# Kernel optimization log

Measured on AMD Instinct MI355X. Metric: run time of the kernel, lower is better.

Reference implementation:

```python
import jax, jax.numpy as jnp
import numpy as np

N_NODES = 100000
N_EDGES = 1000000
IN_F, HID_F, OUT_F = 128, 128, 16


def setup_inputs() -> dict:
    key = jax.random.key(0)
    ks = jax.random.split(key, 8)
    x = jax.random.normal(ks[0], (N_NODES, IN_F), dtype=jnp.float32)
    src = jax.random.randint(ks[1], (N_EDGES,), 0, N_NODES, dtype=jnp.int64)
    dst = jax.random.randint(ks[2], (N_EDGES,), 0, N_NODES, dtype=jnp.int64)
    s = 1.0 / np.sqrt(HID_F)
    W1 = jax.random.normal(ks[3], (IN_F, HID_F), dtype=jnp.float32) * s
    W2 = jax.random.normal(ks[4], (HID_F, HID_F), dtype=jnp.float32) * s
    W3 = jax.random.normal(ks[5], (HID_F, HID_F), dtype=jnp.float32) * s
    W4 = jax.random.normal(ks[6], (HID_F, HID_F), dtype=jnp.float32) * s
    W5 = jax.random.normal(ks[7], (HID_F, OUT_F), dtype=jnp.float32) * s
    return {
        "x": x, "src": src, "dst": dst,
        "W1": W1, "b1": jnp.zeros((HID_F,), jnp.float32),
        "W2": W2, "b2": jnp.zeros((HID_F,), jnp.float32),
        "W3": W3, "b3": jnp.zeros((HID_F,), jnp.float32),
        "W4": W4, "b4": jnp.zeros((HID_F,), jnp.float32),
        "W5": W5, "b5": jnp.zeros((OUT_F,), jnp.float32),
    }


def reference(x, src, dst, W1, b1, W2, b2, W3, b3, W4, b4, W5, b5):
    N = x.shape[0]
    # in-degree per destination node (static graph, computed once)
    deg = jax.ops.segment_sum(jnp.ones_like(dst, dtype=x.dtype), dst, num_segments=N)
    inv = (1.0 / (deg + 1.0))[:, None]  # gcn aggregator normalizer: 1/(deg_in+1)

    def sage_gcn(h, W, b):
        # h_neigh[v] = (h[v] + sum_{u->v} h[u]) / (deg_in(v)+1); then linear
        agg = (h + jax.ops.segment_sum(h[src], dst, num_segments=N)) * inv
        return agg @ W + b

    h = jax.nn.relu(sage_gcn(x, W1, b1))
    h = jax.nn.relu(sage_gcn(h, W2, b2))
    h = jax.nn.relu(sage_gcn(h, W3, b3))
    h = jax.nn.relu(sage_gcn(h, W4, b4))
    h = sage_gcn(h, W5, b5)
    return jax.nn.log_softmax(h, axis=-1)
```

## Files before the change

### kernel.cpp

```cpp
#include <hip/hip_runtime.h>
#include <hip/hip_bf16.h>

#define NNODES 100000
#define NEDGES 1000000
#define HID 128
#define OUTF 16
#define NB 16
#define BCAP 81920
#define KB 64

typedef __attribute__((ext_vector_type(8))) short short8;
typedef __attribute__((ext_vector_type(4))) float floatx4;
typedef unsigned int uint32;
typedef unsigned short ushort16;

__device__ __forceinline__ float blo(uint32 u) { return __uint_as_float(u << 16); }
__device__ __forceinline__ float bhi(uint32 u) { return __uint_as_float(u & 0xffff0000u); }
__device__ __forceinline__ ushort16 f2b(float f) {
    __hip_bfloat16 h = __float2bfloat16(f);
    return *reinterpret_cast<ushort16*>(&h);
}


__global__ __launch_bounds__(256) void bucketize(const int* __restrict__ src,
                                                 const int* __restrict__ dst,
                                                 int* __restrict__ counts,
                                                 int* __restrict__ bcursor,
                                                 int2* __restrict__ stage, int E) {
    __shared__ int cnt[NB];
    __shared__ int base[NB];
    int t = threadIdx.x;
    int e = blockIdx.x * 256 + t;
    if (t < NB) cnt[t] = 0;
    __syncthreads();
    int s = 0, d = 0, b = 0, r = 0;
    bool valid = e < E;
    if (valid) {
        s = src[e];
        d = dst[e];
        atomicAdd(&counts[d], 1);
        b = (int)((unsigned)(d * NB) / (unsigned)NNODES);
        r = atomicAdd(&cnt[b], 1);
    }
    __syncthreads();
    if (t < NB) base[t] = atomicAdd(&bcursor[t], cnt[t]);
    __syncthreads();
    if (valid) {
        int pos = base[b] + r;
        if (pos < BCAP) stage[(size_t)b * BCAP + pos] = make_int2(s, d);
    }
}

__global__ __launch_bounds__(256) void fill2(const int2* __restrict__ stage,
                                             const int* __restrict__ bcursor,
                                             const int* __restrict__ offs,
                                             int* __restrict__ cursor,
                                             int* __restrict__ csr) {
    int blk = blockIdx.x;
    int b = (blk & 7) + 8 * ((blk >> 3) & 1);
    int slot = blk >> 4;
    int cntb = min(bcursor[b], BCAP);
    int per = (cntb + KB - 1) / KB;
    int s0 = slot * per;
    int s1 = min(s0 + per, cntb);
    const int2* st = stage + (size_t)b * BCAP;
    for (int i = s0 + threadIdx.x; i < s1; i += 256) {
        int2 sd = st[i];
        int p = atomicAdd(&cursor[sd.y], 1);
        csr[offs[sd.y] + p] = sd.x;
    }
}

__global__ void scan1(const int* __restrict__ counts, int* __restrict__ offs,
                      int* __restrict__ bsum, int N) {
    __shared__ int tmp[256];
    int t = threadIdx.x;
    int i = blockIdx.x * 256 + t;
    int v = (i < N) ? counts[i] : 0;
    tmp[t] = v;
    __syncthreads();
    for (int d = 1; d < 256; d <<= 1) {
        int add = (t >= d) ? tmp[t - d] : 0;
        __syncthreads();
        tmp[t] += add;
        __syncthreads();
    }
    if (i < N) offs[i] = tmp[t] - v;
    if (t == 255) bsum[blockIdx.x] = tmp[255];
}

__global__ void scan2(int* __restrict__ bsum, int nb) {
    __shared__ int tmp[512];
    int t = threadIdx.x;
    int v = (t < nb) ? bsum[t] : 0;
    tmp[t] = v;
    __syncthreads();
    for (int d = 1; d < 512; d <<= 1) {
        int add = (t >= d) ? tmp[t - d] : 0;
        __syncthreads();
        tmp[t] += add;
        __syncthreads();
    }
    if (t < nb) bsum[t] = tmp[t] - v;
}

__global__ void scan3(int* __restrict__ offs, const int* __restrict__ bsum,
                      const int* __restrict__ counts, float* __restrict__ inv,
                      int N, int E) {
    int i = blockIdx.x * 256 + threadIdx.x;
    if (i < N) {
        offs[i] += bsum[blockIdx.x];
        inv[i] = 1.0f / (float)(counts[i] + 1);
    }
    if (i == 0) offs[N] = E;
}


__global__ void pack_w(const float* __restrict__ W, ushort16* __restrict__ Wp) {
    int b = blockIdx.x;
    int lane = threadIdx.x;
    int nt = b >> 2, ks = b & 3;
    int n = nt * 16 + (lane & 15);
    int kbase = ks * 32 + ((lane >> 4) << 3);
    ushort16 tmp[8];
#pragma unroll
    for (int i = 0; i < 8; i++) tmp[i] = f2b(W[(size_t)(kbase + i) * HID + n]);
    *(uint4*)&Wp[((size_t)b * 64 + lane) * 8] = *(uint4*)tmp;
}


template <int AF32>
__global__ __launch_bounds__(256) void gemm_mfma(const void* __restrict__ Av,
                                                 const ushort16* __restrict__ Wp,
                                                 ushort16* __restrict__ Z, int M) {
    __shared__ __align__(16) ushort16 Wl[32 * 64 * 8];
    int t = threadIdx.x;
    const uint4* wp4 = (const uint4*)Wp;
    uint4* wl4 = (uint4*)Wl;
#pragma unroll
    for (int p = 0; p < 8; p++) wl4[t + p * 256] = wp4[t + p * 256];
    __syncthreads();

    int wv = t >> 6, lane = t & 63;
    int row = blockIdx.x * 64 + wv * 16 + (lane & 15);
    int rowc = min(row, M - 1);
    int kb = (lane >> 4) << 3;

    short8 a[4];
    if (AF32) {
        const float* A = (const float*)Av;
#pragma unroll
        for (int ks = 0; ks < 4; ks++) {
            const float* p = A + (size_t)rowc * HID + ks * 32 + kb;
            floatx4 lo = *(const floatx4*)p;
            floatx4 hi = *(const floatx4*)(p + 4);
            union { short8 s; ushort16 u[8]; } cv;
            cv.u[0] = f2b(lo.x); cv.u[1] = f2b(lo.y); cv.u[2] = f2b(lo.z); cv.u[3] = f2b(lo.w);
            cv.u[4] = f2b(hi.x); cv.u[5] = f2b(hi.y); cv.u[6] = f2b(hi.z); cv.u[7] = f2b(hi.w);
            a[ks] = cv.s;
        }
    } else {
        const ushort16* A = (const ushort16*)Av;
#pragma unroll
        for (int ks = 0; ks < 4; ks++)
            a[ks] = *(const short8*)(A + (size_t)rowc * HID + ks * 32 + kb);
    }

    floatx4 acc[8];
#pragma unroll
    for (int nt = 0; nt < 8; nt++) acc[nt] = (floatx4){0.f, 0.f, 0.f, 0.f};

#pragma unroll
    for (int nt = 0; nt < 8; nt++) {
#pragma unroll
        for (int ks = 0; ks < 4; ks++) {
            short8 b = *(const short8*)&Wl[(size_t)(((nt << 2) | ks) * 64 + lane) * 8];
            acc[nt] = __builtin_amdgcn_mfma_f32_16x16x32_bf16(a[ks], b, acc[nt], 0, 0, 0);
        }
    }

    int orow = blockIdx.x * 64 + wv * 16 + ((lane >> 4) << 2);
    int col = lane & 15;
#pragma unroll
    for (int i = 0; i < 4; i++) {
        int r = orow + i;
        if (r < M) {
#pragma unroll
            for (int nt = 0; nt < 8; nt++)
                Z[(size_t)r * HID + nt * 16 + col] = f2b(acc[nt][i]);
        }
    }
}


__global__ __launch_bounds__(256) void agg_bf16(const uint32* __restrict__ Z,
                                                const int* __restrict__ offs,
                                                const int* __restrict__ csr,
                                                const float* __restrict__ inv,
                                                const float* __restrict__ bias,
                                                uint32* __restrict__ H, int N) {
    int v = (blockIdx.x * blockDim.x + threadIdx.x) >> 6;
    int lane = threadIdx.x & 63;
    if (v >= N) return;
    uint32 sv = Z[(size_t)v * 64 + lane];
    float ax = blo(sv), ay = bhi(sv);
    int beg = offs[v], cnt = offs[v + 1] - beg;
    for (int c0 = 0; c0 < cnt; c0 += 64) {
        int m = min(cnt - c0, 64);
        int idx = (lane < m) ? csr[beg + c0 + lane] : 0;
        int j = 0;
        for (; j + 8 <= m; j += 8) {
            uint32 a[8];
#pragma unroll
            for (int q = 0; q < 8; q++) {
                int u = __builtin_amdgcn_readlane(idx, j + q);
                a[q] = Z[(size_t)u * 64 + lane];
            }
#pragma unroll
            for (int q = 0; q < 8; q++) { ax += blo(a[q]); ay += bhi(a[q]); }
        }
        if (j + 4 <= m) {
            uint32 a[4];
#pragma unroll
            for (int q = 0; q < 4; q++) {
                int u = __builtin_amdgcn_readlane(idx, j + q);
                a[q] = Z[(size_t)u * 64 + lane];
            }
#pragma unroll
            for (int q = 0; q < 4; q++) { ax += blo(a[q]); ay += bhi(a[q]); }
            j += 4;
        }
        for (; j < m; ++j) {
            int u = __builtin_amdgcn_readlane(idx, j);
            uint32 a0 = Z[(size_t)u * 64 + lane];
            ax += blo(a0);
            ay += bhi(a0);
        }
    }
    float sc = inv[v];
    float2 b = *(const float2*)(bias + lane * 2);
    float rx = fmaxf(ax * sc + b.x, 0.f);
    float ry = fmaxf(ay * sc + b.y, 0.f);
    H[(size_t)v * 64 + lane] = (uint32)f2b(rx) | ((uint32)f2b(ry) << 16);
}


__global__ __launch_bounds__(256) void gemm16(const ushort16* __restrict__ A,
                                              const float* __restrict__ W5,
                                              float* __restrict__ Z16, int M) {
    __shared__ float Ws[HID * OUTF];
    int t = threadIdx.x;
    for (int i = t; i < HID * OUTF; i += 256) Ws[i] = W5[i];
    __syncthreads();
    int gid = blockIdx.x * 256 + t;
    int r = gid >> 4, c = gid & 15;
    if (r >= M) return;
    const uint32* a = (const uint32*)(A + (size_t)r * HID);
    float acc = 0.f;
#pragma unroll
    for (int k = 0; k < 64; k += 2) {
        uint32 u0 = a[k], u1 = a[k + 1];
        acc += blo(u0) * Ws[(2 * k + 0) * OUTF + c];
        acc += bhi(u0) * Ws[(2 * k + 1) * OUTF + c];
        acc += blo(u1) * Ws[(2 * k + 2) * OUTF + c];
        acc += bhi(u1) * Ws[(2 * k + 3) * OUTF + c];
    }
    Z16[(size_t)r * OUTF + c] = acc;
}


__global__ __launch_bounds__(256) void agg16_lsm(const float* __restrict__ Z16,
                                                 const int* __restrict__ offs,
                                                 const int* __restrict__ csr,
                                                 const float* __restrict__ inv,
                                                 const float* __restrict__ b5,
                                                 float* __restrict__ out, int N) {
    int gid = blockIdx.x * 256 + threadIdx.x;
    int v = gid >> 4, c = gid & 15;
    if (v >= N) return;
    int beg = offs[v], cnt = offs[v + 1] - beg;
    float acc = Z16[(size_t)v * OUTF + c];
    for (int c0 = 0; c0 < cnt; c0 += 16) {
        int m = min(cnt - c0, 16);
        int idx = (c < m) ? csr[beg + c0 + c] : 0;
        int j = 0;
        for (; j + 4 <= m; j += 4) {
            int u0 = __shfl(idx, j, 16);
            int u1 = __shfl(idx, j + 1, 16);
            int u2 = __shfl(idx, j + 2, 16);
            int u3 = __shfl(idx, j + 3, 16);
            float a0 = Z16[(size_t)u0 * OUTF + c];
            float a1 = Z16[(size_t)u1 * OUTF + c];
            float a2 = Z16[(size_t)u2 * OUTF + c];
            float a3 = Z16[(size_t)u3 * OUTF + c];
            acc += a0 + a1 + a2 + a3;
        }
        for (; j < m; ++j) {
            int u = __shfl(idx, j, 16);
            acc += Z16[(size_t)u * OUTF + c];
        }
    }
    float val = acc * inv[v] + b5[c];
    float m = val;
#pragma unroll
    for (int d = 1; d < 16; d <<= 1) m = fmaxf(m, __shfl_xor(m, d));
    float e = expf(val - m);
    float ssum = e;
#pragma unroll
    for (int d = 1; d < 16; d <<= 1) ssum += __shfl_xor(ssum, d);
    out[(size_t)v * OUTF + c] = val - m - logf(ssum);
}


extern "C" void kernel_launch(void* const* d_in, const int* in_sizes, int n_in,
                              void* d_out, int out_size, void* d_ws, size_t ws_size,
                              hipStream_t stream) {
    const float* x   = (const float*)d_in[0];
    const int*   src = (const int*)d_in[1];
    const int*   dst = (const int*)d_in[2];
    const float* W1 = (const float*)d_in[3];
    const float* b1 = (const float*)d_in[4];
    const float* W2 = (const float*)d_in[5];
    const float* b2 = (const float*)d_in[6];
    const float* W3 = (const float*)d_in[7];
    const float* b3 = (const float*)d_in[8];
    const float* W4 = (const float*)d_in[9];
    const float* b4 = (const float*)d_in[10];
    const float* W5 = (const float*)d_in[11];
    const float* b5 = (const float*)d_in[12];

    char* ws = (char*)d_ws;
    size_t off = 0;
    auto alloc = [&](size_t bytes) {
        void* p = ws + off;
        off = (off + bytes + 255) & ~(size_t)255;
        return p;
    };
    ushort16* zb   = (ushort16*)alloc((size_t)NNODES * HID * 2);
    ushort16* hb   = (ushort16*)alloc((size_t)NNODES * HID * 2);
    float*    z16f = (float*)alloc((size_t)NNODES * OUTF * 4);
    int*      counts = (int*)alloc((size_t)NNODES * 4);
    int*      offs   = (int*)alloc((size_t)(NNODES + 1) * 4);
    int*      bsum   = (int*)alloc(512 * 4);
    int*      csr    = (int*)alloc((size_t)NEDGES * 4);
    float*    invd   = (float*)alloc((size_t)NNODES * 4);
    int2*     stage  = (int2*)alloc((size_t)NB * BCAP * 8);
    int*      bcursor = (int*)alloc(NB * 4);
    ushort16* Wp1 = (ushort16*)alloc((size_t)HID * HID * 2);
    ushort16* Wp2 = (ushort16*)alloc((size_t)HID * HID * 2);
    ushort16* Wp3 = (ushort16*)alloc((size_t)HID * HID * 2);
    ushort16* Wp4 = (ushort16*)alloc((size_t)HID * HID * 2);
    (void)ws_size; (void)in_sizes; (void)n_in; (void)out_size;

    const int N = NNODES, E = NEDGES;
    int nb = (N + 255) / 256;

    hipMemsetAsync(counts, 0, (size_t)N * 4, stream);
    hipMemsetAsync(bcursor, 0, NB * 4, stream);
    bucketize<<<(E + 255) / 256, 256, 0, stream>>>(src, dst, counts, bcursor, stage, E);
    scan1<<<nb, 256, 0, stream>>>(counts, offs, bsum, N);
    scan2<<<1, 512, 0, stream>>>(bsum, nb);
    scan3<<<nb, 256, 0, stream>>>(offs, bsum, counts, invd, N, E);
    hipMemsetAsync(counts, 0, (size_t)N * 4, stream);
    fill2<<<NB * KB, 256, 0, stream>>>(stage, bcursor, offs, counts, csr);

    pack_w<<<32, 64, 0, stream>>>(W1, Wp1);
    pack_w<<<32, 64, 0, stream>>>(W2, Wp2);
    pack_w<<<32, 64, 0, stream>>>(W3, Wp3);
    pack_w<<<32, 64, 0, stream>>>(W4, Wp4);

    int gemmGrid = (N + 63) / 64;
    int aggGrid  = (N + 3) / 4;

    gemm_mfma<1><<<gemmGrid, 256, 0, stream>>>((const void*)x, Wp1, zb, N);
    agg_bf16<<<aggGrid, 256, 0, stream>>>((const uint32*)zb, offs, csr, invd, b1, (uint32*)hb, N);

    gemm_mfma<0><<<gemmGrid, 256, 0, stream>>>((const void*)hb, Wp2, zb, N);
    agg_bf16<<<aggGrid, 256, 0, stream>>>((const uint32*)zb, offs, csr, invd, b2, (uint32*)hb, N);

    gemm_mfma<0><<<gemmGrid, 256, 0, stream>>>((const void*)hb, Wp3, zb, N);
    agg_bf16<<<aggGrid, 256, 0, stream>>>((const uint32*)zb, offs, csr, invd, b3, (uint32*)hb, N);

    gemm_mfma<0><<<gemmGrid, 256, 0, stream>>>((const void*)hb, Wp4, zb, N);
    agg_bf16<<<aggGrid, 256, 0, stream>>>((const uint32*)zb, offs, csr, invd, b4, (uint32*)hb, N);

    gemm16<<<(N * OUTF + 255) / 256, 256, 0, stream>>>(hb, W5, z16f, N);
    agg16_lsm<<<(N * OUTF + 255) / 256, 256, 0, stream>>>(z16f, offs, csr, invd, b5,
                                                          (float*)d_out, N);
}
```

Baseline: 411.0 us.

## Slice hidden features into column blocks, fuse CSR rank, bf16 final layer

Hidden activations are stored as eight 16-column slices of all nodes. Each aggregation block gathers from one 32-byte-per-node slice, which shrinks the working set per pass and is meant to improve L2 hit rates during the random neighbor gathers. CSR construction now records each edge's rank from the counting atomic, which removes the second memset and the cursor atomics in fill, and bucketize stages edges through LDS so its stores are coalesced. The final 16-wide layer keeps its intermediate in bf16 with two columns per thread and adds nontemporal loads and stores, trading some precision for less memory traffic.

```diff
diff --git a/kernel.cpp b/kernel.cpp
--- a/kernel.cpp
+++ b/kernel.cpp
@@ -8,10 +8,13 @@
 #define NB 16
 #define BCAP 81920
 #define KB 64
+#define BZT 1024
+#define AGG_BN 128
 
 typedef __attribute__((ext_vector_type(8))) short short8;
 typedef __attribute__((ext_vector_type(4))) float floatx4;
 typedef unsigned int uint32;
+typedef unsigned long long ull;
 typedef unsigned short ushort16;
 
 __device__ __forceinline__ float blo(uint32 u) { return __uint_as_float(u << 16); }
@@ -20,41 +23,62 @@
     __hip_bfloat16 h = __float2bfloat16(f);
     return *reinterpret_cast<ushort16*>(&h);
 }
-
-
-__global__ __launch_bounds__(256) void bucketize(const int* __restrict__ src,
+__device__ __forceinline__ uint32 pack2(float a, float b) {
+    return (uint32)f2b(a) | ((uint32)f2b(b) << 16);
+}
+
+
+__global__ __launch_bounds__(BZT) void bucketize(const int* __restrict__ src,
                                                  const int* __restrict__ dst,
                                                  int* __restrict__ counts,
                                                  int* __restrict__ bcursor,
-                                                 int2* __restrict__ stage, int E) {
-    __shared__ int cnt[NB];
-    __shared__ int base[NB];
-    int t = threadIdx.x;
-    int e = blockIdx.x * 256 + t;
+                                                 ull* __restrict__ stage, int E) {
+    __shared__ int cnt[NB], lbase[NB], gbase[NB];
+    __shared__ int2 buf[BZT];
+    __shared__ unsigned char bb[BZT];
+    int t = threadIdx.x;
+    int e0 = blockIdx.x * BZT;
+    int e = e0 + t;
     if (t < NB) cnt[t] = 0;
     __syncthreads();
-    int s = 0, d = 0, b = 0, r = 0;
+    int s = 0; unsigned y = 0; int b = 0, r = 0;
     bool valid = e < E;
     if (valid) {
         s = src[e];
-        d = dst[e];
-        atomicAdd(&counts[d], 1);
-        b = (int)((unsigned)(d * NB) / (unsigned)NNODES);
+        int d = dst[e];
+        int rk = atomicAdd(&counts[d], 1);
+        y = (unsigned)d | ((unsigned)rk << 17);
+        b = (int)((unsigned)d * NB / NNODES);
         r = atomicAdd(&cnt[b], 1);
     }
     __syncthreads();
-    if (t < NB) base[t] = atomicAdd(&bcursor[t], cnt[t]);
+    if (t == 0) {
+        int run = 0;
+        for (int i = 0; i < NB; i++) { lbase[i] = run; run += cnt[i]; }
+    }
     __syncthreads();
     if (valid) {
-        int pos = base[b] + r;
-        if (pos < BCAP) stage[(size_t)b * BCAP + pos] = make_int2(s, d);
-    }
-}
-
-__global__ __launch_bounds__(256) void fill2(const int2* __restrict__ stage,
+        int p = lbase[b] + r;
+        buf[p] = make_int2(s, (int)y);
+        bb[p] = (unsigned char)b;
+    }
+    if (t < NB) gbase[t] = atomicAdd(&bcursor[t], cnt[t]);
+    __syncthreads();
+    int nvalid = min(BZT, E - e0);
+    if (t < nvalid) {
+        int b2 = bb[t];
+        int2 sd = buf[t];
+        int pos = gbase[b2] + (t - lbase[b2]);
+        if (pos < BCAP) {
+            ull val = (ull)(unsigned)sd.x | ((ull)(unsigned)sd.y << 32);
+            __builtin_nontemporal_store(val, &stage[(size_t)b2 * BCAP + pos]);
+        }
+    }
+}
+
+__global__ __launch_bounds__(256) void fill2(const ull* __restrict__ stage,
                                              const int* __restrict__ bcursor,
                                              const int* __restrict__ offs,
-                                             int* __restrict__ cursor,
                                              int* __restrict__ csr) {
     int blk = blockIdx.x;
     int b = (blk & 7) + 8 * ((blk >> 3) & 1);
@@ -63,11 +87,14 @@
     int per = (cntb + KB - 1) / KB;
     int s0 = slot * per;
     int s1 = min(s0 + per, cntb);
-    const int2* st = stage + (size_t)b * BCAP;
+    const ull* st = stage + (size_t)b * BCAP;
     for (int i = s0 + threadIdx.x; i < s1; i += 256) {
-        int2 sd = st[i];
-        int p = atomicAdd(&cursor[sd.y], 1);
-        csr[offs[sd.y] + p] = sd.x;
+        ull v = __builtin_nontemporal_load(&st[i]);
+        int s = (int)(v & 0xffffffffu);
+        unsigned y = (unsigned)(v >> 32);
+        int d = (int)(y & 0x1ffffu);
+        int r = (int)(y >> 17);
+        csr[offs[d] + r] = s;
     }
 }
 
@@ -161,9 +188,12 @@
         }
     } else {
         const ushort16* A = (const ushort16*)Av;
-#pragma unroll
-        for (int ks = 0; ks < 4; ks++)
-            a[ks] = *(const short8*)(A + (size_t)rowc * HID + ks * 32 + kb);
+        int sl = kb >> 4, soff = kb & 8;
+#pragma unroll
+        for (int ks = 0; ks < 4; ks++) {
+            int slice = ks * 2 + sl;
+            a[ks] = *(const short8*)(A + ((size_t)slice * NNODES + rowc) * 16 + soff);
+        }
     }
 
     floatx4 acc[8];
@@ -187,128 +217,129 @@
         if (r < M) {
 #pragma unroll
             for (int nt = 0; nt < 8; nt++)
-                Z[(size_t)r * HID + nt * 16 + col] = f2b(acc[nt][i]);
-        }
-    }
-}
-
-
-__global__ __launch_bounds__(256) void agg_bf16(const uint32* __restrict__ Z,
-                                                const int* __restrict__ offs,
-                                                const int* __restrict__ csr,
-                                                const float* __restrict__ inv,
-                                                const float* __restrict__ bias,
-                                                uint32* __restrict__ H, int N) {
-    int v = (blockIdx.x * blockDim.x + threadIdx.x) >> 6;
-    int lane = threadIdx.x & 63;
-    if (v >= N) return;
-    uint32 sv = Z[(size_t)v * 64 + lane];
-    float ax = blo(sv), ay = bhi(sv);
-    int beg = offs[v], cnt = offs[v + 1] - beg;
-    for (int c0 = 0; c0 < cnt; c0 += 64) {
-        int m = min(cnt - c0, 64);
-        int idx = (lane < m) ? csr[beg + c0 + lane] : 0;
-        int j = 0;
-        for (; j + 8 <= m; j += 8) {
-            uint32 a[8];
+                Z[((size_t)nt * NNODES + r) * 16 + col] = f2b(acc[nt][i]);
+        }
+    }
+}
+
+
+__global__ __launch_bounds__(256) void agg_sliced(const uint32* __restrict__ Z,
+                                                  const int* __restrict__ offs,
+                                                  const int* __restrict__ csr,
+                                                  const float* __restrict__ inv,
+                                                  const float* __restrict__ bias,
+                                                  uint32* __restrict__ H, int N) {
+    int s = blockIdx.x & 7;
+    int chunk = blockIdx.x >> 3;
+    int t = threadIdx.x;
+    int grp = t >> 3;
+    int l4 = t & 7;
+    int lanebase = t & 56;
+    const uint32* Zs = Z + (size_t)s * NNODES * 8;
+    uint32* Hs = H + (size_t)s * NNODES * 8;
+    const float2* bs = (const float2*)(bias + s * 16);
+    float2 bb = bs[l4];
+#pragma unroll
+    for (int it = 0; it < AGG_BN / 32; ++it) {
+        int v = chunk * AGG_BN + it * 32 + grp;
+        bool act = v < N;
+        float ax = 0.f, ay = 0.f, iv = 0.f;
+        int beg = 0, cnt = 0;
+        if (act) {
+            uint32 sv = Zs[(size_t)v * 8 + l4];
+            ax = blo(sv); ay = bhi(sv);
+            beg = offs[v];
+            cnt = offs[v + 1] - beg;
+            iv = inv[v];
+        }
+        for (int j = 0; j < cnt; j += 8) {
+            int m = min(cnt - j, 8);
+            int idxr = 0;
+            if (l4 < m) idxr = __builtin_nontemporal_load(&csr[beg + j + l4]);
 #pragma unroll
             for (int q = 0; q < 8; q++) {
-                int u = __builtin_amdgcn_readlane(idx, j + q);
-                a[q] = Z[(size_t)u * 64 + lane];
+                if (q < m) {
+                    int u = __shfl(idxr, lanebase + q, 64);
+                    uint32 g = Zs[(size_t)u * 8 + l4];
+                    ax += blo(g); ay += bhi(g);
+                }
             }
-#pragma unroll
-            for (int q = 0; q < 8; q++) { ax += blo(a[q]); ay += bhi(a[q]); }
-        }
-        if (j + 4 <= m) {
-            uint32 a[4];
-#pragma unroll
-            for (int q = 0; q < 4; q++) {
-                int u = __builtin_amdgcn_readlane(idx, j + q);
-                a[q] = Z[(size_t)u * 64 + lane];
-            }
-#pragma unroll
-            for (int q = 0; q < 4; q++) { ax += blo(a[q]); ay += bhi(a[q]); }
-            j += 4;
-        }
-        for (; j < m; ++j) {
-            int u = __builtin_amdgcn_readlane(idx, j);
-            uint32 a0 = Z[(size_t)u * 64 + lane];
-            ax += blo(a0);
-            ay += bhi(a0);
-        }
-    }
-    float sc = inv[v];
-    float2 b = *(const float2*)(bias + lane * 2);
-    float rx = fmaxf(ax * sc + b.x, 0.f);
-    float ry = fmaxf(ay * sc + b.y, 0.f);
-    H[(size_t)v * 64 + lane] = (uint32)f2b(rx) | ((uint32)f2b(ry) << 16);
-}
-
-
-__global__ __launch_bounds__(256) void gemm16(const ushort16* __restrict__ A,
+        }
+        if (act) {
+            float rx = fmaxf(ax * iv + bb.x, 0.f);
+            float ry = fmaxf(ay * iv + bb.y, 0.f);
+            __builtin_nontemporal_store(pack2(rx, ry), &Hs[(size_t)v * 8 + l4]);
+        }
+    }
+}
+
+
+__global__ __launch_bounds__(256) void gemm16(const uint32* __restrict__ A,
                                               const float* __restrict__ W5,
-                                              float* __restrict__ Z16, int M) {
+                                              uint32* __restrict__ Z16, int M) {
     __shared__ float Ws[HID * OUTF];
     int t = threadIdx.x;
     for (int i = t; i < HID * OUTF; i += 256) Ws[i] = W5[i];
     __syncthreads();
     int gid = blockIdx.x * 256 + t;
-    int r = gid >> 4, c = gid & 15;
+    int r = gid >> 3, cp = gid & 7;
     if (r >= M) return;
-    const uint32* a = (const uint32*)(A + (size_t)r * HID);
-    float acc = 0.f;
-#pragma unroll
-    for (int k = 0; k < 64; k += 2) {
-        uint32 u0 = a[k], u1 = a[k + 1];
-        acc += blo(u0) * Ws[(2 * k + 0) * OUTF + c];
-        acc += bhi(u0) * Ws[(2 * k + 1) * OUTF + c];
-        acc += blo(u1) * Ws[(2 * k + 2) * OUTF + c];
-        acc += bhi(u1) * Ws[(2 * k + 3) * OUTF + c];
-    }
-    Z16[(size_t)r * OUTF + c] = acc;
-}
-
-
-__global__ __launch_bounds__(256) void agg16_lsm(const float* __restrict__ Z16,
+    float a0 = 0.f, a1 = 0.f;
+#pragma unroll
+    for (int s8 = 0; s8 < 8; s8++) {
+        const uint32* ar = A + ((size_t)s8 * NNODES + r) * 8;
+#pragma unroll
+        for (int k = 0; k < 8; k++) {
+            uint32 u = ar[k];
+            float f0 = blo(u), f1 = bhi(u);
+            a0 += f0 * Ws[(s8 * 16 + 2 * k) * OUTF + 2 * cp] +
+                  f1 * Ws[(s8 * 16 + 2 * k + 1) * OUTF + 2 * cp];
+            a1 += f0 * Ws[(s8 * 16 + 2 * k) * OUTF + 2 * cp + 1] +
+                  f1 * Ws[(s8 * 16 + 2 * k + 1) * OUTF + 2 * cp + 1];
+        }
+    }
+    Z16[(size_t)r * 8 + cp] = pack2(a0, a1);
+}
+
+
+__global__ __launch_bounds__(256) void agg16_lsm(const uint32* __restrict__ Z16,
                                                  const int* __restrict__ offs,
                                                  const int* __restrict__ csr,
                                                  const float* __restrict__ inv,
                                                  const float* __restrict__ b5,
                                                  float* __restrict__ out, int N) {
     int gid = blockIdx.x * 256 + threadIdx.x;
-    int v = gid >> 4, c = gid & 15;
+    int v = gid >> 3, l = gid & 7;
     if (v >= N) return;
+    int lanebase = threadIdx.x & 56;
+    uint32 sv = Z16[(size_t)v * 8 + l];
+    float ax = blo(sv), ay = bhi(sv);
     int beg = offs[v], cnt = offs[v + 1] - beg;
-    float acc = Z16[(size_t)v * OUTF + c];
-    for (int c0 = 0; c0 < cnt; c0 += 16) {
-        int m = min(cnt - c0, 16);
-        int idx = (c < m) ? csr[beg + c0 + c] : 0;
-        int j = 0;
-        for (; j + 4 <= m; j += 4) {
-            int u0 = __shfl(idx, j, 16);
-            int u1 = __shfl(idx, j + 1, 16);
-            int u2 = __shfl(idx, j + 2, 16);
-            int u3 = __shfl(idx, j + 3, 16);
-            float a0 = Z16[(size_t)u0 * OUTF + c];
-            float a1 = Z16[(size_t)u1 * OUTF + c];
-            float a2 = Z16[(size_t)u2 * OUTF + c];
-            float a3 = Z16[(size_t)u3 * OUTF + c];
-            acc += a0 + a1 + a2 + a3;
-        }
-        for (; j < m; ++j) {
-            int u = __shfl(idx, j, 16);
-            acc += Z16[(size_t)u * OUTF + c];
-        }
-    }
-    float val = acc * inv[v] + b5[c];
-    float m = val;
-#pragma unroll
-    for (int d = 1; d < 16; d <<= 1) m = fmaxf(m, __shfl_xor(m, d));
-    float e = expf(val - m);
-    float ssum = e;
-#pragma unroll
-    for (int d = 1; d < 16; d <<= 1) ssum += __shfl_xor(ssum, d);
-    out[(size_t)v * OUTF + c] = val - m - logf(ssum);
+    for (int j = 0; j < cnt; j += 8) {
+        int m = min(cnt - j, 8);
+        int idxr = 0;
+        if (l < m) idxr = __builtin_nontemporal_load(&csr[beg + j + l]);
+#pragma unroll
+        for (int q = 0; q < 8; q++) {
+            if (q < m) {
+                int u = __shfl(idxr, lanebase + q, 64);
+                uint32 g = Z16[(size_t)u * 8 + l];
+                ax += blo(g); ay += bhi(g);
+            }
+        }
+    }
+    float iv = inv[v];
+    float2 bb = *(const float2*)(b5 + 2 * l);
+    float vx = ax * iv + bb.x, vy = ay * iv + bb.y;
+    float mm = fmaxf(vx, vy);
+#pragma unroll
+    for (int d = 1; d < 8; d <<= 1) mm = fmaxf(mm, __shfl_xor(mm, d, 8));
+    float ex = expf(vx - mm), ey = expf(vy - mm);
+    float ss = ex + ey;
+#pragma unroll
+    for (int d = 1; d < 8; d <<= 1) ss += __shfl_xor(ss, d, 8);
+    float ls = logf(ss);
+    *(float2*)&out[(size_t)v * OUTF + 2 * l] = make_float2(vx - mm - ls, vy - mm - ls);
 }
 
 
@@ -338,13 +369,13 @@
     };
     ushort16* zb   = (ushort16*)alloc((size_t)NNODES * HID * 2);
     ushort16* hb   = (ushort16*)alloc((size_t)NNODES * HID * 2);
-    float*    z16f = (float*)alloc((size_t)NNODES * OUTF * 4);
+    uint32*   z16b = (uint32*)alloc((size_t)NNODES * OUTF * 2);
     int*      counts = (int*)alloc((size_t)NNODES * 4);
     int*      offs   = (int*)alloc((size_t)(NNODES + 1) * 4);
     int*      bsum   = (int*)alloc(512 * 4);
     int*      csr    = (int*)alloc((size_t)NEDGES * 4);
     float*    invd   = (float*)alloc((size_t)NNODES * 4);
-    int2*     stage  = (int2*)alloc((size_t)NB * BCAP * 8);
+    ull*      stage  = (ull*)alloc((size_t)NB * BCAP * 8);
     int*      bcursor = (int*)alloc(NB * 4);
     ushort16* Wp1 = (ushort16*)alloc((size_t)HID * HID * 2);
     ushort16* Wp2 = (ushort16*)alloc((size_t)HID * HID * 2);
@@ -357,12 +388,11 @@
 
     hipMemsetAsync(counts, 0, (size_t)N * 4, stream);
     hipMemsetAsync(bcursor, 0, NB * 4, stream);
-    bucketize<<<(E + 255) / 256, 256, 0, stream>>>(src, dst, counts, bcursor, stage, E);
+    bucketize<<<(E + BZT - 1) / BZT, BZT, 0, stream>>>(src, dst, counts, bcursor, stage, E);
     scan1<<<nb, 256, 0, stream>>>(counts, offs, bsum, N);
     scan2<<<1, 512, 0, stream>>>(bsum, nb);
     scan3<<<nb, 256, 0, stream>>>(offs, bsum, counts, invd, N, E);
-    hipMemsetAsync(counts, 0, (size_t)N * 4, stream);
-    fill2<<<NB * KB, 256, 0, stream>>>(stage, bcursor, offs, counts, csr);
+    fill2<<<NB * KB, 256, 0, stream>>>(stage, bcursor, offs, csr);
 
     pack_w<<<32, 64, 0, stream>>>(W1, Wp1);
     pack_w<<<32, 64, 0, stream>>>(W2, Wp2);
@@ -370,21 +400,21 @@
     pack_w<<<32, 64, 0, stream>>>(W4, Wp4);
 
     int gemmGrid = (N + 63) / 64;
-    int aggGrid  = (N + 3) / 4;
+    int aggGrid  = 8 * ((N + AGG_BN - 1) / AGG_BN);
 
     gemm_mfma<1><<<gemmGrid, 256, 0, stream>>>((const void*)x, Wp1, zb, N);
-    agg_bf16<<<aggGrid, 256, 0, stream>>>((const uint32*)zb, offs, csr, invd, b1, (uint32*)hb, N);
+    agg_sliced<<<aggGrid, 256, 0, stream>>>((const uint32*)zb, offs, csr, invd, b1, (uint32*)hb, N);
 
     gemm_mfma<0><<<gemmGrid, 256, 0, stream>>>((const void*)hb, Wp2, zb, N);
-    agg_bf16<<<aggGrid, 256, 0, stream>>>((const uint32*)zb, offs, csr, invd, b2, (uint32*)hb, N);
+    agg_sliced<<<aggGrid, 256, 0, stream>>>((const uint32*)zb, offs, csr, invd, b2, (uint32*)hb, N);
 
     gemm_mfma<0><<<gemmGrid, 256, 0, stream>>>((const void*)hb, Wp3, zb, N);
-    agg_bf16<<<aggGrid, 256, 0, stream>>>((const uint32*)zb, offs, csr, invd, b3, (uint32*)hb, N);
+    agg_sliced<<<aggGrid, 256, 0, stream>>>((const uint32*)zb, offs, csr, invd, b3, (uint32*)hb, N);
 
     gemm_mfma<0><<<gemmGrid, 256, 0, stream>>>((const void*)hb, Wp4, zb, N);
-    agg_bf16<<<aggGrid, 256, 0, stream>>>((const uint32*)zb, offs, csr, invd, b4, (uint32*)hb, N);
-
-    gemm16<<<(N * OUTF + 255) / 256, 256, 0, stream>>>(hb, W5, z16f, N);
-    agg16_lsm<<<(N * OUTF + 255) / 256, 256, 0, stream>>>(z16f, offs, csr, invd, b5,
-                                                          (float*)d_out, N);
-}
+    agg_sliced<<<aggGrid, 256, 0, stream>>>((const uint32*)zb, offs, csr, invd, b4, (uint32*)hb, N);
+
+    gemm16<<<(N * 8 + 255) / 256, 256, 0, stream>>>((const uint32*)hb, W5, z16b, N);
+    agg16_lsm<<<(N * 8 + 255) / 256, 256, 0, stream>>>(z16b, offs, csr, invd, b5,
+                                                       (float*)d_out, N);
+}
```

Measured after the change: 636.9 us. 1.55x slower.
